# Kernel tuning notes

Measured on AMD Instinct MI355X. Metric: run time of the kernel, lower is better.

## Reference

```python
import jax, jax.numpy as jnp
import numpy as np

K = 4            # number of expert kernels
TEMPERATURE = 30.0  # T_max, initial temperature
KS = 3
PAD = 1
STRIDE = 1


def setup_inputs() -> dict:
    key = jax.random.key(0)
    k1, k2, k3, k4, k5 = jax.random.split(key, 5)
    b, c_in, c_out, f, t, ctx = 32, 256, 256, 64, 64, 256
    x = jax.random.normal(k1, (b, c_in, f, t), dtype=jnp.float32)
    g = jax.random.normal(k2, (b, ctx), dtype=jnp.float32)
    # expert kernels: (k, out, in//groups, ks, ks), kaiming-normal-ish init
    fan_in = c_in * KS * KS
    weight = jax.random.normal(k3, (K, c_out, c_in, KS, KS), dtype=jnp.float32) * jnp.sqrt(2.0 / fan_in)
    # attention Dense: ctx -> k * att_groups (att_groups = 1)
    dense_w = jax.random.normal(k4, (ctx, K), dtype=jnp.float32) * jnp.sqrt(1.0 / ctx)
    dense_b = jnp.zeros((K,), dtype=jnp.float32)
    return {"x": x, "g": g, "weight": weight, "dense_w": dense_w, "dense_b": dense_b}


def reference(x, g, weight, dense_w, dense_b):
    b, c, f, t = x.shape
    k, c_out, c_in_pg, ks, _ = weight.shape
    # attention over k expert kernels, per batch element (att_groups = 1)
    logits = g @ dense_w + dense_b                      # (b, k)
    attention = jax.nn.softmax(logits / TEMPERATURE, axis=-1)
    # per-sample mixed kernel: (b, out, in, ks, ks)
    agg_w = jnp.einsum('bk,koihw->boihw', attention, weight)
    agg_w = agg_w.reshape(b * c_out, c_in_pg, ks, ks)
    # batched per-sample conv via feature_group_count = groups * b (groups = 1)
    xg = x.reshape(1, b * c, f, t)
    out = jax.lax.conv_general_dilated(
        xg, agg_w,
        window_strides=(STRIDE, STRIDE),
        padding=((PAD, PAD), (PAD, PAD)),
        lhs_dilation=(1, 1), rhs_dilation=(1, 1),
        dimension_numbers=('NCHW', 'OIHW', 'NCHW'),
        feature_group_count=b,
    )
    return out.reshape(b, c_out, out.shape[-2], out.shape[-1])
```

## Files before the change

kernel.cpp:

```cpp
#include <hip/hip_runtime.h>
#include <hip/hip_bf16.h>
#include <stdint.h>

#define BATCH 32
#define CIN   256
#define COUT  256
#define FH    64
#define FW    64
#define NK    4
#define CTX   256
#define TEMP  30.0f

typedef __attribute__((ext_vector_type(8))) short bf16x8;
typedef __attribute__((ext_vector_type(4))) float f32x4;

__device__ __forceinline__ unsigned short f2bf(float f) {
    union { float f; uint32_t u; } a; a.f = f;
    uint32_t r = a.u + 0x7fffu + ((a.u >> 16) & 1u);
    return (unsigned short)(r >> 16);
}

#define WMIX_OFF  1024
#define WMIX_BYTES (32u * 9u * 8u * 4u * 256u * 16u)
#define XP_OFF    (WMIX_OFF + WMIX_BYTES)

__global__ __launch_bounds__(256, 2) void prep_kernel(
        const float* __restrict__ weight,
        const float* __restrict__ g,
        const float* __restrict__ dw,
        const float* __restrict__ db,
        uint32_t* __restrict__ wmix,
        const float* __restrict__ x,
        uint32_t* __restrict__ xp) {
    __shared__ __align__(16) char LDSU[73856];
    __shared__ float logit_s[8];
    __shared__ float att_s[8];

    const int bid = blockIdx.x;
    const int t   = threadIdx.x;

    if (bid < 512) {
        short* S = (short*)LDSU;
        const int cog = bid & 31;
        const int bg  = bid >> 5;
        const int co0 = cog * 8;
        const int b0  = bg * 2;
        const size_t EST = (size_t)COUT * CIN * 9;

        {
            const int p  = t >> 5;
            const int i0 = t & 31;
            const int nb = p >> 2, k = p & 3;
            const float* gp = g + (size_t)(b0 + nb) * CTX;
            float part = 0.f;
#pragma unroll
            for (int j = 0; j < 8; ++j) {
                const int i = i0 + j * 32;
                part += gp[i] * dw[i * NK + k];
            }
#pragma unroll
            for (int m = 1; m <= 16; m <<= 1) part += __shfl_xor(part, m);
            if (i0 == 0) logit_s[p] = part + db[k];
        }
        __syncthreads();
        if (t < 8) {
            const int nb = t >> 2;
            const float l0 = logit_s[nb * 4 + 0] * (1.f / TEMP);
            const float l1 = logit_s[nb * 4 + 1] * (1.f / TEMP);
            const float l2 = logit_s[nb * 4 + 2] * (1.f / TEMP);
            const float l3 = logit_s[nb * 4 + 3] * (1.f / TEMP);
            const float m  = fmaxf(fmaxf(l0, l1), fmaxf(l2, l3));
            const float e0 = expf(l0 - m), e1 = expf(l1 - m);
            const float e2 = expf(l2 - m), e3 = expf(l3 - m);
            const float s  = e0 + e1 + e2 + e3;
            const int   k  = t & 3;
            const float e  = (k == 0) ? e0 : (k == 1) ? e1 : (k == 2) ? e2 : e3;
            att_s[t] = e / s;
        }
        __syncthreads();

        float a[2][4];
#pragma unroll
        for (int nb = 0; nb < 2; ++nb)
#pragma unroll
            for (int k = 0; k < 4; ++k)
                a[nb][k] = att_s[nb * 4 + k];

        const int co_l  = t >> 5;
        const int inner = t & 31;
        const float* wbase = weight + (size_t)(co0 + co_l) * 2304;

#pragma unroll 2
        for (int i = 0; i < 18; ++i) {
            const int e4 = inner + 32 * i;
            float4 w[4];
#pragma unroll
            for (int k = 0; k < 4; ++k)
                w[k] = *(const float4*)(wbase + k * EST + (size_t)e4 * 4);
#pragma unroll
            for (int nb = 0; nb < 2; ++nb) {
                float mx = a[nb][0] * w[0].x + a[nb][1] * w[1].x + a[nb][2] * w[2].x + a[nb][3] * w[3].x;
                float my = a[nb][0] * w[0].y + a[nb][1] * w[1].y + a[nb][2] * w[2].y + a[nb][3] * w[3].y;
                float mz = a[nb][0] * w[0].z + a[nb][1] * w[1].z + a[nb][2] * w[2].z + a[nb][3] * w[3].z;
                float mw = a[nb][0] * w[0].w + a[nb][1] * w[1].w + a[nb][2] * w[2].w + a[nb][3] * w[3].w;
                uint32_t lo = (uint32_t)f2bf(mx) | ((uint32_t)f2bf(my) << 16);
                uint32_t hi = (uint32_t)f2bf(mz) | ((uint32_t)f2bf(mw) << 16);
                uint2* d = (uint2*)(S + ((nb * 8 + co_l) * 2308 + e4 * 4));
                *d = make_uint2(lo, hi);
            }
        }
        __syncthreads();

        const int co_w = t & 7;
        const int slot = t >> 3;
#pragma unroll 2
        for (int j = 0; j < 18; ++j) {
            const int GG  = j * 32 + slot;
            const int b_l = (GG >= 288) ? 1 : 0;
            const int rem = GG - b_l * 288;
            const int tap = rem >> 5;
            const int ch  = (rem >> 2) & 7;
            const int q   = rem & 3;
            const short* sp = S + (b_l * 8 + co_w) * 2308;
            const int ebase = (ch * 32 + q * 8) * 9 + tap;
            uint32_t d[4];
#pragma unroll
            for (int rp = 0; rp < 4; ++rp) {
                uint32_t lo = (uint16_t)sp[ebase + (2 * rp) * 9];
                uint32_t hi = (uint16_t)sp[ebase + (2 * rp + 1) * 9];
                d[rp] = lo | (hi << 16);
            }
            uint32_t* dst = wmix +
                ((((size_t)((b0 + b_l) * 9 + tap) * 8 + ch) * 4 + q) * 256 + co0 + co_w) * 4;
            *(uint4*)dst = make_uint4(d[0], d[1], d[2], d[3]);
        }
    } else {
        uint32_t* P = (uint32_t*)LDSU;
        const int idx = bid - 512;
        const int yg  = idx % 11;
        const int rem = idx / 11;
        const int ch  = rem & 7;
        const int b   = rem >> 3;

        for (int i = t; i < 6 * 1088; i += 256) P[i] = 0;
        __syncthreads();

        const int ci_l = t >> 3;
        const int col0 = (t & 7) * 8;
        const int q = ci_l >> 3, r = ci_l & 7;
        unsigned short* Ps = (unsigned short*)P;

#pragma unroll
        for (int yy = 0; yy < 6; ++yy) {
            const int y = yg * 6 + yy;
            if (y >= 1 && y <= 64) {
                const float* xr = x + (((size_t)(b * 256 + ch * 32 + ci_l) * 64) + (y - 1)) * 64 + col0;
                float4 v0 = *(const float4*)xr;
                float4 v1 = *(const float4*)(xr + 4);
                unsigned short bf[8];
                bf[0] = f2bf(v0.x); bf[1] = f2bf(v0.y); bf[2] = f2bf(v0.z); bf[3] = f2bf(v0.w);
                bf[4] = f2bf(v1.x); bf[5] = f2bf(v1.y); bf[6] = f2bf(v1.z); bf[7] = f2bf(v1.w);
#pragma unroll
                for (int j = 0; j < 8; ++j)
                    Ps[yy * 2176 + (q * 68 + (col0 + j + 1)) * 8 + r] = bf[j];
            }
        }
        __syncthreads();

        const int qo = t >> 6, l = t & 63;
#pragma unroll
        for (int yy = 0; yy < 6; ++yy) {
            const int y = yg * 6 + yy;
            uint32_t* base = xp + (((((size_t)(b * 8 + ch) * 4 + qo) * 66) + y) * 68) * 4;
#pragma unroll
            for (int i = 0; i < 4; ++i)
                base[l + i * 64] = P[yy * 1088 + qo * 272 + l + i * 64];
            if (l < 16) base[l + 256] = P[yy * 1088 + qo * 272 + l + 256];
        }
    }
}

__global__ __launch_bounds__(256, 3) void conv_mfma(
        const char* __restrict__ xp,
        const char* __restrict__ wmix,
        float* __restrict__ out) {
    const int tid  = threadIdx.x;
    const int lane = tid & 63;
    const int wv   = tid >> 6;
    const int wm   = wv & 1;
    const int wn   = wv >> 1;
    const int l4   = lane >> 4;
    const int m16  = lane & 15;

    const int bx  = blockIdx.x;
    const int wid = (bx & 7) * 256 + (bx >> 3);
    const int ptile = wid & 31;
    const int coT   = (wid >> 5) & 1;
    const int b     = wid >> 6;
    const int y0    = ptile * 2;

    const char* wmix_b = wmix + (size_t)b * 9 * 8 * 4 * 256 * 16;
    const char* xp_b   = xp + (size_t)b * 8 * 4 * 66 * 68 * 16;

    f32x4 acc[4][4];
#pragma unroll
    for (int i = 0; i < 4; ++i)
#pragma unroll
        for (int j = 0; j < 4; ++j)
            acc[i][j] = (f32x4){0.f, 0.f, 0.f, 0.f};

    const char* Abase = wmix_b + (size_t)l4 * 4096
                      + (size_t)(coT * 128 + wm * 64 + m16) * 16;
    const int yout = y0 + wn;

#pragma unroll 1
    for (int ch = 0; ch < 8; ++ch) {
#pragma unroll
        for (int dy = 0; dy < 3; ++dy) {
            const char* Ap = Abase + (size_t)ch * 16384 + (size_t)(dy * 3) * 131072;
            const char* Bp = xp_b
                + (((size_t)(ch * 4 + l4)) * 66 + (yout + dy)) * 1088 + m16 * 16;
#pragma unroll
            for (int dx = 0; dx < 3; ++dx) {
                bf16x8 a[4], bb[4];
#pragma unroll
                for (int sm = 0; sm < 4; ++sm)
                    a[sm] = *(const bf16x8*)(Ap + dx * 131072 + sm * 256);
#pragma unroll
                for (int sn = 0; sn < 4; ++sn)
                    bb[sn] = *(const bf16x8*)(Bp + dx * 16 + sn * 256);
                __builtin_amdgcn_s_setprio(1);
#pragma unroll
                for (int sm = 0; sm < 4; ++sm)
#pragma unroll
                    for (int sn = 0; sn < 4; ++sn)
                        acc[sm][sn] = __builtin_amdgcn_mfma_f32_16x16x32_bf16(
                            a[sm], bb[sn], acc[sm][sn], 0, 0, 0);
                __builtin_amdgcn_s_setprio(0);
            }
        }
    }

#pragma unroll
    for (int sm = 0; sm < 4; ++sm) {
#pragma unroll
        for (int sn = 0; sn < 4; ++sn) {
#pragma unroll
            for (int r = 0; r < 4; ++r) {
                const int co = coT * 128 + wm * 64 + sm * 16 + l4 * 4 + r;
                const int xx = sn * 16 + m16;
                out[(((size_t)b * COUT + co) * FH + yout) * FW + xx] = acc[sm][sn][r];
            }
        }
    }
}

extern "C" void kernel_launch(void* const* d_in, const int* in_sizes, int n_in,
                              void* d_out, int out_size, void* d_ws, size_t ws_size,
                              hipStream_t stream) {
    const float* x       = (const float*)d_in[0];
    const float* g       = (const float*)d_in[1];
    const float* weight  = (const float*)d_in[2];
    const float* dense_w = (const float*)d_in[3];
    const float* dense_b = (const float*)d_in[4];
    float* out = (float*)d_out;

    uint32_t* wmix = (uint32_t*)((char*)d_ws + WMIX_OFF);
    uint32_t* xp   = (uint32_t*)((char*)d_ws + XP_OFF);

    prep_kernel<<<3328, 256, 0, stream>>>(weight, g, dense_w, dense_b, wmix, x, xp);
    conv_mfma<<<2048, 256, 0, stream>>>((const char*)xp, (const char*)wmix, out);
}
```

Measured before the change: 444.7 us.

## Stage conv operands in LDS via direct global-to-LDS loads and rework prep blocks

The conv kernel now uses 2 waves per block and loads weight and input tiles into LDS with global_load_lds. Each wave then computes 64 output channels across 2 output rows (4x8 MFMA tiles) instead of reading operands straight from global memory. The prep kernel halves the per-block channel tile for weight mixing and drops the LDS transpose for input padding, writing bf16 pairs directly. The aim is to cut redundant global and L2 traffic and raise occupancy, at the cost of extra barriers, unpipelined loads per (ch,dy) step, and uncoalesced scalar reads of x in prep.

```diff
diff --git a/kernel.cpp b/kernel.cpp
--- a/kernel.cpp
+++ b/kernel.cpp
@@ -24,7 +24,7 @@
 #define WMIX_BYTES (32u * 9u * 8u * 4u * 256u * 16u)
 #define XP_OFF    (WMIX_OFF + WMIX_BYTES)
 
-__global__ __launch_bounds__(256, 2) void prep_kernel(
+__global__ __launch_bounds__(256) void prep_kernel(
         const float* __restrict__ weight,
         const float* __restrict__ g,
         const float* __restrict__ dw,
@@ -32,18 +32,17 @@
         uint32_t* __restrict__ wmix,
         const float* __restrict__ x,
         uint32_t* __restrict__ xp) {
-    __shared__ __align__(16) char LDSU[73856];
+    __shared__ __align__(16) short S[2 * 4 * 2308];
     __shared__ float logit_s[8];
     __shared__ float att_s[8];
 
     const int bid = blockIdx.x;
     const int t   = threadIdx.x;
 
-    if (bid < 512) {
-        short* S = (short*)LDSU;
-        const int cog = bid & 31;
-        const int bg  = bid >> 5;
-        const int co0 = cog * 8;
+    if (bid < 1024) {
+        const int cog = bid & 63;
+        const int bg  = bid >> 6;
+        const int co0 = cog * 4;
         const int b0  = bg * 2;
         const size_t EST = (size_t)COUT * CIN * 9;
 
@@ -86,13 +85,13 @@
             for (int k = 0; k < 4; ++k)
                 a[nb][k] = att_s[nb * 4 + k];
 
-        const int co_l  = t >> 5;
-        const int inner = t & 31;
+        const int co_l  = t >> 6;
+        const int inner = t & 63;
         const float* wbase = weight + (size_t)(co0 + co_l) * 2304;
 
-#pragma unroll 2
-        for (int i = 0; i < 18; ++i) {
-            const int e4 = inner + 32 * i;
+#pragma unroll 3
+        for (int i = 0; i < 9; ++i) {
+            const int e4 = inner + 64 * i;
             float4 w[4];
 #pragma unroll
             for (int k = 0; k < 4; ++k)
@@ -105,23 +104,23 @@
                 float mw = a[nb][0] * w[0].w + a[nb][1] * w[1].w + a[nb][2] * w[2].w + a[nb][3] * w[3].w;
                 uint32_t lo = (uint32_t)f2bf(mx) | ((uint32_t)f2bf(my) << 16);
                 uint32_t hi = (uint32_t)f2bf(mz) | ((uint32_t)f2bf(mw) << 16);
-                uint2* d = (uint2*)(S + ((nb * 8 + co_l) * 2308 + e4 * 4));
+                uint2* d = (uint2*)(S + ((nb * 4 + co_l) * 2308 + e4 * 4));
                 *d = make_uint2(lo, hi);
             }
         }
         __syncthreads();
 
-        const int co_w = t & 7;
-        const int slot = t >> 3;
-#pragma unroll 2
-        for (int j = 0; j < 18; ++j) {
-            const int GG  = j * 32 + slot;
+        const int co_w = t & 3;
+        const int slot = t >> 2;
+#pragma unroll 3
+        for (int j = 0; j < 9; ++j) {
+            const int GG  = j * 64 + slot;
             const int b_l = (GG >= 288) ? 1 : 0;
             const int rem = GG - b_l * 288;
             const int tap = rem >> 5;
             const int ch  = (rem >> 2) & 7;
             const int q   = rem & 3;
-            const short* sp = S + (b_l * 8 + co_w) * 2308;
+            const short* sp = S + (b_l * 4 + co_w) * 2308;
             const int ebase = (ch * 32 + q * 8) * 9 + tap;
             uint32_t d[4];
 #pragma unroll
@@ -135,62 +134,57 @@
             *(uint4*)dst = make_uint4(d[0], d[1], d[2], d[3]);
         }
     } else {
-        uint32_t* P = (uint32_t*)LDSU;
-        const int idx = bid - 512;
-        const int yg  = idx % 11;
-        const int rem = idx / 11;
-        const int ch  = rem & 7;
-        const int b   = rem >> 3;
-
-        for (int i = t; i < 6 * 1088; i += 256) P[i] = 0;
-        __syncthreads();
-
-        const int ci_l = t >> 3;
-        const int col0 = (t & 7) * 8;
-        const int q = ci_l >> 3, r = ci_l & 7;
-        unsigned short* Ps = (unsigned short*)P;
-
-#pragma unroll
-        for (int yy = 0; yy < 6; ++yy) {
-            const int y = yg * 6 + yy;
-            if (y >= 1 && y <= 64) {
-                const float* xr = x + (((size_t)(b * 256 + ch * 32 + ci_l) * 64) + (y - 1)) * 64 + col0;
-                float4 v0 = *(const float4*)xr;
-                float4 v1 = *(const float4*)(xr + 4);
-                unsigned short bf[8];
-                bf[0] = f2bf(v0.x); bf[1] = f2bf(v0.y); bf[2] = f2bf(v0.z); bf[3] = f2bf(v0.w);
-                bf[4] = f2bf(v1.x); bf[5] = f2bf(v1.y); bf[6] = f2bf(v1.z); bf[7] = f2bf(v1.w);
-#pragma unroll
-                for (int j = 0; j < 8; ++j)
-                    Ps[yy * 2176 + (q * 68 + (col0 + j + 1)) * 8 + r] = bf[j];
-            }
-        }
-        __syncthreads();
-
-        const int qo = t >> 6, l = t & 63;
-#pragma unroll
-        for (int yy = 0; yy < 6; ++yy) {
-            const int y = yg * 6 + yy;
-            uint32_t* base = xp + (((((size_t)(b * 8 + ch) * 4 + qo) * 66) + y) * 68) * 4;
-#pragma unroll
-            for (int i = 0; i < 4; ++i)
-                base[l + i * 64] = P[yy * 1088 + qo * 272 + l + i * 64];
-            if (l < 16) base[l + 256] = P[yy * 1088 + qo * 272 + l + 256];
+        const int idx  = bid - 1024;
+        const int b    = idx / 48;
+        const int rem2 = idx % 48;
+        const int ch   = rem2 / 6;
+        const int yg   = rem2 % 6;
+
+        const int q    = t >> 6;
+        const int id64 = t & 63;
+
+        for (int yy = 0; yy < 11; ++yy) {
+            const int y = yg * 11 + yy;
+            uint32_t* base = xp + (((size_t)(b * 8 + ch) * 4 + q) * 66 + y) * 272;
+            if (y == 0 || y == 65) {
+#pragma unroll
+                for (int i = 0; i < 4; ++i) base[id64 + i * 64] = 0;
+                if (id64 < 16) base[256 + id64] = 0;
+            } else {
+#pragma unroll
+                for (int i = 0; i < 5; ++i) {
+                    const int d = id64 + i * 64;
+                    if (i == 4 && d >= 272) break;
+                    if (d < 272) {
+                        const int col = d >> 2, rp = d & 3;
+                        uint32_t v = 0;
+                        if (col >= 1 && col <= 64) {
+                            const int ci = ch * 32 + q * 8 + rp * 2;
+                            const float* p = x + ((size_t)(b * 256 + ci) * 64 + (y - 1)) * 64 + (col - 1);
+                            v = (uint32_t)f2bf(p[0]) | ((uint32_t)f2bf(p[4096]) << 16);
+                        }
+                        base[d] = v;
+                    }
+                }
+            }
         }
     }
 }
 
-__global__ __launch_bounds__(256, 3) void conv_mfma(
+__global__ __launch_bounds__(128, 2) void conv_mfma(
         const char* __restrict__ xp,
         const char* __restrict__ wmix,
         float* __restrict__ out) {
+    __shared__ __align__(16) char As[3 * 8192];
+    __shared__ __align__(16) char Bs[2 * 4352];
+
     const int tid  = threadIdx.x;
     const int lane = tid & 63;
     const int wv   = tid >> 6;
-    const int wm   = wv & 1;
-    const int wn   = wv >> 1;
     const int l4   = lane >> 4;
     const int m16  = lane & 15;
+    const int sl_co = lane >> 2;
+    const int sl_q  = lane & 3;
 
     const int bx  = blockIdx.x;
     const int wid = (bx & 7) * 256 + (bx >> 3);
@@ -202,38 +196,73 @@
     const char* wmix_b = wmix + (size_t)b * 9 * 8 * 4 * 256 * 16;
     const char* xp_b   = xp + (size_t)b * 8 * 4 * 66 * 68 * 16;
 
-    f32x4 acc[4][4];
+    f32x4 acc[4][8];
 #pragma unroll
     for (int i = 0; i < 4; ++i)
 #pragma unroll
-        for (int j = 0; j < 4; ++j)
+        for (int j = 0; j < 8; ++j)
             acc[i][j] = (f32x4){0.f, 0.f, 0.f, 0.f};
 
-    const char* Abase = wmix_b + (size_t)l4 * 4096
-                      + (size_t)(coT * 128 + wm * 64 + m16) * 16;
-    const int yout = y0 + wn;
+    const int aOff = wv * 4096 + m16 * 64 + l4 * 16;
+    const int bOff = m16 * 64 + l4 * 16;
 
 #pragma unroll 1
     for (int ch = 0; ch < 8; ++ch) {
-#pragma unroll
+#pragma unroll 1
         for (int dy = 0; dy < 3; ++dy) {
-            const char* Ap = Abase + (size_t)ch * 16384 + (size_t)(dy * 3) * 131072;
-            const char* Bp = xp_b
-                + (((size_t)(ch * 4 + l4)) * 66 + (yout + dy)) * 1088 + m16 * 16;
+            __syncthreads();
+#pragma unroll
+            for (int i = 0; i < 12; ++i) {
+                const int s  = wv + i * 2;
+                const int dx = s >> 3;
+                const int cog = s & 7;
+                const char* gsrc = wmix_b
+                    + ((size_t)((dy * 3 + dx) * 8 + ch) * 4 + sl_q) * 4096
+                    + (coT * 128 + cog * 16 + sl_co) * 16;
+                char* ldst = (char*)As + dx * 8192 + cog * 1024 + lane * 16;
+                __builtin_amdgcn_global_load_lds(
+                    (const __attribute__((address_space(1))) void*)gsrc,
+                    (__attribute__((address_space(3))) void*)ldst, 16, 0, 0);
+            }
+            {
+                const int yb = y0 + dy + wv;
+                const char* grow = xp_b + ((size_t)ch * 4) * 71808 + (size_t)yb * 1088;
+                char* lrow = (char*)Bs + wv * 4352;
+#pragma unroll
+                for (int c0 = 0; c0 < 4; ++c0) {
+                    const char* gsrc = grow + (size_t)sl_q * 71808 + (c0 * 16 + sl_co) * 16;
+                    char* ldst = lrow + c0 * 1024 + lane * 16;
+                    __builtin_amdgcn_global_load_lds(
+                        (const __attribute__((address_space(1))) void*)gsrc,
+                        (__attribute__((address_space(3))) void*)ldst, 16, 0, 0);
+                }
+                if (lane < 16) {
+                    const char* gsrc = grow + (size_t)sl_q * 71808 + (64 + sl_co) * 16;
+                    char* ldst = lrow + 4096 + lane * 16;
+                    __builtin_amdgcn_global_load_lds(
+                        (const __attribute__((address_space(1))) void*)gsrc,
+                        (__attribute__((address_space(3))) void*)ldst, 16, 0, 0);
+                }
+            }
+            __syncthreads();
+
 #pragma unroll
             for (int dx = 0; dx < 3; ++dx) {
-                bf16x8 a[4], bb[4];
+                bf16x8 a[4], bb[8];
 #pragma unroll
                 for (int sm = 0; sm < 4; ++sm)
-                    a[sm] = *(const bf16x8*)(Ap + dx * 131072 + sm * 256);
-#pragma unroll
-                for (int sn = 0; sn < 4; ++sn)
-                    bb[sn] = *(const bf16x8*)(Bp + dx * 16 + sn * 256);
+                    a[sm] = *(const bf16x8*)((const char*)As + dx * 8192 + sm * 1024 + aOff);
+#pragma unroll
+                for (int rr = 0; rr < 2; ++rr)
+#pragma unroll
+                    for (int sn = 0; sn < 4; ++sn)
+                        bb[rr * 4 + sn] = *(const bf16x8*)((const char*)Bs
+                            + rr * 4352 + sn * 1024 + dx * 64 + bOff);
                 __builtin_amdgcn_s_setprio(1);
 #pragma unroll
                 for (int sm = 0; sm < 4; ++sm)
 #pragma unroll
-                    for (int sn = 0; sn < 4; ++sn)
+                    for (int sn = 0; sn < 8; ++sn)
                         acc[sm][sn] = __builtin_amdgcn_mfma_f32_16x16x32_bf16(
                             a[sm], bb[sn], acc[sm][sn], 0, 0, 0);
                 __builtin_amdgcn_s_setprio(0);
@@ -244,12 +273,16 @@
 #pragma unroll
     for (int sm = 0; sm < 4; ++sm) {
 #pragma unroll
-        for (int sn = 0; sn < 4; ++sn) {
-#pragma unroll
-            for (int r = 0; r < 4; ++r) {
-                const int co = coT * 128 + wm * 64 + sm * 16 + l4 * 4 + r;
-                const int xx = sn * 16 + m16;
-                out[(((size_t)b * COUT + co) * FH + yout) * FW + xx] = acc[sm][sn][r];
+        for (int rr = 0; rr < 2; ++rr) {
+#pragma unroll
+            for (int sn = 0; sn < 4; ++sn) {
+#pragma unroll
+                for (int r = 0; r < 4; ++r) {
+                    const int co = coT * 128 + wv * 64 + sm * 16 + l4 * 4 + r;
+                    const int y  = y0 + rr;
+                    const int xx = sn * 16 + m16;
+                    out[(((size_t)b * COUT + co) * FH + y) * FW + xx] = acc[sm][rr * 4 + sn][r];
+                }
             }
         }
     }
@@ -268,6 +301,6 @@
     uint32_t* wmix = (uint32_t*)((char*)d_ws + WMIX_OFF);
     uint32_t* xp   = (uint32_t*)((char*)d_ws + XP_OFF);
 
-    prep_kernel<<<3328, 256, 0, stream>>>(weight, g, dense_w, dense_b, wmix, x, xp);
-    conv_mfma<<<2048, 256, 0, stream>>>((const char*)xp, (const char*)wmix, out);
+    prep_kernel<<<2560, 256, 0, stream>>>(weight, g, dense_w, dense_b, wmix, x, xp);
+    conv_mfma<<<2048, 128, 0, stream>>>((const char*)xp, (const char*)wmix, out);
 }
```

New measurement: 471.2 us. +6.0%, slower.
